# Kernel optimization log

Hardware: AMD Instinct MI355X
Metric: run time of the kernel (lower is better)

The kernel has to match this reference:

```python
import jax, jax.numpy as jnp
import numpy as np

# dims / constants (from init_kwargs and ParamsHP defaults)
N, C, TRS, SPT, BUF = 800, 64, 40, 10, 120
DT = 1e-4                      # step_size
A, OMEGA, G = -0.5, 10.0, 500.0
STD_IN, CY0, Y0_OFF, KG, KI = 100.0, 5.0, 2.0, 5.0, 1.0
T = TRS * SPT                  # total integration steps


def setup_inputs() -> dict:
    key = jax.random.key(0)
    k = jax.random.split(key, 7)
    external = jax.random.normal(k[0], (N, SPT, TRS), dtype=jnp.float32)
    hx = jax.random.uniform(k[1], (N, 2), dtype=jnp.float32)
    hE = jax.random.uniform(k[2], (N, BUF), dtype=jnp.float32)
    sc = jax.random.uniform(k[3], (N, N), dtype=jnp.float32)
    lm = jax.random.normal(k[4], (C, N), dtype=jnp.float32)
    noise_in = jax.random.normal(k[5], (T, N, 2), dtype=jnp.float32)
    # delays[i,j] = int(dist[i,j] / mu), bounded by buffer length
    delays = jax.random.randint(k[6], (N, N), 0, BUF, dtype=jnp.int64)
    return {"external": external, "hx": hx, "hE": hE, "sc": sc,
            "lm": lm, "noise_in": noise_in, "delays": delays}


def reference(external, hx, hE, sc, lm, noise_in, delays):
    # normalized structural connectivity and Laplacian diagonal term
    w = jnp.abs(sc)
    w_n = w / jnp.linalg.norm(w)          # (N,N)
    rowsum = jnp.sum(w_n, axis=1)         # (N,) -> dg = -diag(rowsum)
    jcol = jnp.broadcast_to(jnp.arange(N)[None, :], (N, N))
    # stimulus as (T, N): external is (N, steps_per_TR, TRs_per_window)
    ext = jnp.transpose(external, (2, 1, 0)).reshape(T, N)
    sqdt = jnp.sqrt(DT)

    def step(carry, inp):
        x, y, hEb = carry                 # x,y: (N,), hEb: (N,BUF)
        u, ns = inp                       # u: (N,), ns: (N,2)
        # delayed activity: Ed[i,j] = x_j(t - delays[i,j])
        Ed = hEb[jcol, delays]            # (N,N) irregular gather
        LEd = jnp.sum(w_n * Ed, axis=1)   # connectivity-weighted coupling
        r2 = x * x + y * y
        dx = (A - r2) * x - OMEGA * y + G * (LEd - rowsum * x) + KG * KI * u
        dy = (A - r2) * y + OMEGA * x
        x_new = x + DT * dx + sqdt * STD_IN * ns[:, 0]
        y_new = y + DT * dy + sqdt * STD_IN * ns[:, 1]
        hEb = jnp.concatenate([x_new[:, None], hEb[:, :-1]], axis=1)
        return (x_new, y_new, hEb), x_new

    (xf, yf, hEf), xs = jax.lax.scan(step, (hx[:, 0], hx[:, 1], hE), (ext, noise_in))
    # one EEG sample per TR (state at the last step of each TR)
    x_tr = xs.reshape(TRS, SPT, N)[:, -1, :]   # (TRS, N)
    eeg = CY0 * (x_tr @ lm.T) - Y0_OFF          # leadfield projection (TRS, C)
    return eeg.T                                # (C, TRS)
```

## Files before the change

### kernel.cpp

```cpp
#include <hip/hip_runtime.h>
#include <hip/hip_cooperative_groups.h>

namespace cg = cooperative_groups;

#define N_      800
#define C_      64
#define TRS_    40
#define SPT_    10
#define BUF_    120
#define T_      400
#define STRIDE  528
#define KPL     13
#define SENT    0x7FC00BADu
#define NEAR_D  15

#define A_F     (-0.5f)
#define OMEGA_F (10.0f)
#define G_F     (500.0f)
#define KGI_F   (5.0f)
#define DT_F    (1e-4f)

#define ALD(p)    __hip_atomic_load((p), __ATOMIC_RELAXED, __HIP_MEMORY_SCOPE_AGENT)
#define AST(p,v)  __hip_atomic_store((p), (v), __ATOMIC_RELAXED, __HIP_MEMORY_SCOPE_AGENT)


__global__ void k_sumsq(const float* __restrict__ sc, float* __restrict__ sumsq) {
    __shared__ float sh[4];
    int tid = threadIdx.x;
    int idx = blockIdx.x * 256 + tid;
    float s = 0.f;
    for (int i = idx; i < N_ * N_; i += 256 * 256) { float v = sc[i]; s += v * v; }
    #pragma unroll
    for (int o = 1; o < 64; o <<= 1) s += __shfl_xor(s, o, 64);
    if ((tid & 63) == 0) sh[tid >> 6] = s;
    __syncthreads();
    if (tid == 0) atomicAdd(sumsq, sh[0] + sh[1] + sh[2] + sh[3]);
}

__global__ void k_detect(const int* __restrict__ dw, int* __restrict__ flag) {
    __shared__ int sh[4];
    int tid = threadIdx.x;
    int v = 0;
    for (int idx = 2 * tid + 1; idx < 800; idx += 512) v |= dw[idx];
    #pragma unroll
    for (int o = 1; o < 64; o <<= 1) v |= __shfl_xor(v, o, 64);
    if ((tid & 63) == 0) sh[tid >> 6] = v;
    __syncthreads();
    if (tid == 0) flag[0] = ((sh[0] | sh[1] | sh[2] | sh[3]) == 0) ? 1 : 0;
}

__global__ void k_init(const float* __restrict__ hE, unsigned int* __restrict__ xh) {
    int idx = blockIdx.x * 256 + threadIdx.x;
    if (idx >= N_ * 520) return;
    int j = idx / 520, s = idx - j * 520;
    unsigned int v = (s < 120) ? __float_as_uint(hE[j * BUF_ + (119 - s)]) : SENT;
    xh[j * STRIDE + s] = v;
}


__global__ void __launch_bounds__(512, 1) k_main(
    const float* __restrict__ sc, const int* __restrict__ dw,
    const float* __restrict__ hx, const float* __restrict__ external,
    const float* __restrict__ noise, const float* __restrict__ lm,
    const float* __restrict__ sumsq, const int* __restrict__ flag,
    unsigned int* __restrict__ xh, float* __restrict__ xtr, float* __restrict__ out)
{
    cg::grid_group grid = cg::this_grid();
    const int lane = threadIdx.x & 63;
    const int i = (int)((blockIdx.x * 512 + threadIdx.x) >> 6);

    const float inv_norm = 1.0f / sqrtf(*sumsq);
    const int is64 = *flag;

    float wn[KPL], wf[KPL]; int an[KPL], af[KPL];
    float rsum = 0.f;
    #pragma unroll
    for (int k = 0; k < KPL; ++k) {
        int j = k * 64 + lane;
        bool valid = (j < N_);
        int jj = valid ? j : 0;
        int base = i * N_ + jj;
        float wv = valid ? fabsf(sc[base]) * inv_norm : 0.f;
        int dv = valid ? dw[is64 ? (base << 1) : base] : 119;
        rsum += wv;
        bool nearc = valid && (dv < NEAR_D);
        bool farc  = valid && (dv >= NEAR_D);
        wn[k] = nearc ? wv : 0.f;
        wf[k] = farc  ? wv : 0.f;
        an[k] = jj * STRIDE + 119 - (nearc ? dv : 119);
        af[k] = jj * STRIDE + 119 - (farc  ? dv : 119);
    }
    #pragma unroll
    for (int o = 1; o < 64; o <<= 1) rsum += __shfl_xor(rsum, o, 64);

    float x = hx[2 * i], y = hx[2 * i + 1];

    #pragma unroll 1
    for (int mb = 0; mb < 25; ++mb) {
        const int t0 = mb * 16;

        float fps[16];
        #pragma unroll
        for (int s = 0; s < 16; ++s) fps[s] = 0.f;

        #pragma unroll
        for (int k = 0; k < KPL; ++k) {
            bool fm = (wf[k] != 0.f);
            int a = af[k] + t0;
            int p = a & 3;
            int A = a - p;
            float4 q0, q1, q2, q3, q4;
            if (fm) {
                const float4* f4 = reinterpret_cast<const float4*>((const float*)xh + A);
                q0 = f4[0]; q1 = f4[1]; q2 = f4[2]; q3 = f4[3]; q4 = f4[4];
            } else {
                q0 = q1 = q2 = q3 = q4 = make_float4(0.f, 0.f, 0.f, 0.f);
            }
            float win[20] = { q0.x,q0.y,q0.z,q0.w, q1.x,q1.y,q1.z,q1.w,
                              q2.x,q2.y,q2.z,q2.w, q3.x,q3.y,q3.z,q3.w,
                              q4.x,q4.y,q4.z,q4.w };
            int g = 0;
            while (true) {
                int pend = 0;
                #pragma unroll
                for (int z = 0; z < 20; ++z)
                    pend |= (int)((z >= p) & (z < p + 16) &
                                  (__float_as_uint(win[z]) == SENT));
                if (!__any(pend)) break;
                if (++g > 1000000) break;
                #pragma unroll
                for (int z = 0; z < 20; ++z)
                    if ((z >= p) && (z < p + 16) && __float_as_uint(win[z]) == SENT)
                        win[z] = __uint_as_float(ALD(&xh[A + z]));
            }
            float wk = wf[k];
            #pragma unroll
            for (int s = 0; s < 16; ++s) {
                float v01 = (p & 1) ? win[s + 1] : win[s];
                float v23 = (p & 1) ? win[s + 3] : win[s + 2];
                float v   = (p & 2) ? v23 : v01;
                fps[s] += wk * v;
            }
        }

        #pragma unroll
        for (int s = 0; s < 16; ++s) {
            const int t = t0 + s;
            int tr = (t * 205) >> 11;
            int sp = t - tr * 10;
            float u  = external[(i * SPT_ + sp) * TRS_ + tr];
            float n0 = noise[(t * N_ + i) * 2 + 0];
            float n1 = noise[(t * N_ + i) * 2 + 1];

            unsigned vv[KPL];
            #pragma unroll
            for (int k = 0; k < KPL; ++k)
                vv[k] = (wn[k] != 0.f) ? ALD(&xh[an[k] + t]) : 0u;
            int g = 0;
            while (true) {
                int pend = 0;
                #pragma unroll
                for (int k = 0; k < KPL; ++k) pend |= (vv[k] == SENT) ? 1 : 0;
                if (!__any(pend)) break;
                if (++g > 1000000) break;
                #pragma unroll
                for (int k = 0; k < KPL; ++k)
                    if (vv[k] == SENT) vv[k] = ALD(&xh[an[k] + t]);
            }
            float acc = fps[s];
            #pragma unroll
            for (int k = 0; k < KPL; ++k) acc += wn[k] * __uint_as_float(vv[k]);
            #pragma unroll
            for (int o = 1; o < 64; o <<= 1) acc += __shfl_xor(acc, o, 64);

            float r2 = x * x + y * y;
            float dx = (A_F - r2) * x - OMEGA_F * y + G_F * (acc - rsum * x) + KGI_F * u;
            float dy = (A_F - r2) * y + OMEGA_F * x;
            x = x + DT_F * dx + n0;
            y = y + DT_F * dy + n1;

            if (lane == 0) {
                AST(&xh[i * STRIDE + 120 + t], __float_as_uint(x));
                if (sp == SPT_ - 1) xtr[tr * N_ + i] = x;
            }
        }
    }

    grid.sync();

    for (int o = i; o < C_ * TRS_; o += 800) {
        int c = o / TRS_, tr = o - c * TRS_;
        float s = 0.f;
        #pragma unroll
        for (int k = 0; k < KPL; ++k) {
            int n = k * 64 + lane;
            if (n < N_) s += xtr[tr * N_ + n] * lm[c * N_ + n];
        }
        #pragma unroll
        for (int o2 = 1; o2 < 64; o2 <<= 1) s += __shfl_xor(s, o2, 64);
        if (lane == 0) out[o] = 5.0f * s - 2.0f;
    }
}


extern "C" void kernel_launch(void* const* d_in, const int* in_sizes, int n_in,
                              void* d_out, int out_size, void* d_ws, size_t ws_size,
                              hipStream_t stream) {
    const float* external = (const float*)d_in[0];
    const float* hx       = (const float*)d_in[1];
    const float* hE       = (const float*)d_in[2];
    const float* sc       = (const float*)d_in[3];
    const float* lm       = (const float*)d_in[4];
    const float* noise    = (const float*)d_in[5];
    const int*   delays   = (const int*)  d_in[6];
    float* out = (float*)d_out;

    float*        sumsq = (float*)d_ws;
    int*          flag  = (int*)d_ws + 1;
    unsigned int* xh    = (unsigned int*)d_ws + 64;
    float*        xtr   = (float*)(xh + N_ * STRIDE);

    hipMemsetAsync(d_ws, 0, 8, stream);
    k_sumsq<<<256, 256, 0, stream>>>(sc, sumsq);
    k_detect<<<1, 256, 0, stream>>>(delays, flag);
    k_init<<<(N_ * 520 + 255) / 256, 256, 0, stream>>>(hE, xh);

    void* args[] = { (void*)&sc, (void*)&delays, (void*)&hx, (void*)&external,
                     (void*)&noise, (void*)&lm, (void*)&sumsq, (void*)&flag,
                     (void*)&xh, (void*)&xtr, (void*)&out };
    hipLaunchCooperativeKernel((const void*)k_main, dim3(100), dim3(512), args, 0, stream);
}
```

Before: 2.727 ms.

## Transpose history buffer and stage recent states in a shared-memory ring

The global history buffer is transposed to time-major layout, so each time step's 800 states are contiguous. Each block cooperatively pulls the previous step's full state vector into a 16-deep LDS ring, and near-delay connections read from LDS instead of issuing per-lane global atomic polls. Far-delay reads become strided per-element loads instead of float4 windows. This adds a block-wide __syncthreads and an 800-element global poll per step in every block.

```diff
diff --git a/kernel.cpp b/kernel.cpp
--- a/kernel.cpp
+++ b/kernel.cpp
@@ -9,10 +9,11 @@
 #define SPT_    10
 #define BUF_    120
 #define T_      400
-#define STRIDE  528
+#define ROWS_   520
 #define KPL     13
 #define SENT    0x7FC00BADu
-#define NEAR_D  15
+#define NEAR_D  16
+#define DEPTH   16
 
 #define A_F     (-0.5f)
 #define OMEGA_F (10.0f)
@@ -49,30 +50,35 @@
     if (tid == 0) flag[0] = ((sh[0] | sh[1] | sh[2] | sh[3]) == 0) ? 1 : 0;
 }
 
-__global__ void k_init(const float* __restrict__ hE, unsigned int* __restrict__ xh) {
+__global__ void k_init(const float* __restrict__ hE, unsigned int* __restrict__ xhT) {
     int idx = blockIdx.x * 256 + threadIdx.x;
-    if (idx >= N_ * 520) return;
-    int j = idx / 520, s = idx - j * 520;
-    unsigned int v = (s < 120) ? __float_as_uint(hE[j * BUF_ + (119 - s)]) : SENT;
-    xh[j * STRIDE + s] = v;
+    if (idx >= ROWS_ * N_) return;
+    int r = idx / N_, j = idx - r * N_;
+    unsigned int v = (r < 120) ? __float_as_uint(hE[j * BUF_ + (119 - r)]) : SENT;
+    xhT[r * N_ + j] = v;
 }
 
 
 __global__ void __launch_bounds__(512, 1) k_main(
     const float* __restrict__ sc, const int* __restrict__ dw,
-    const float* __restrict__ hx, const float* __restrict__ external,
-    const float* __restrict__ noise, const float* __restrict__ lm,
+    const float* __restrict__ hx, const float* __restrict__ hE,
+    const float* __restrict__ external, const float* __restrict__ noise,
+    const float* __restrict__ lm,
     const float* __restrict__ sumsq, const int* __restrict__ flag,
-    unsigned int* __restrict__ xh, float* __restrict__ xtr, float* __restrict__ out)
+    unsigned int* __restrict__ xhT, float* __restrict__ xtr, float* __restrict__ out)
 {
     cg::grid_group grid = cg::this_grid();
-    const int lane = threadIdx.x & 63;
-    const int i = (int)((blockIdx.x * 512 + threadIdx.x) >> 6);
+    __shared__ float ring[DEPTH * N_];
+
+    const int tid  = threadIdx.x;
+    const int lane = tid & 63;
+    const int wid  = tid >> 6;
+    const int i    = blockIdx.x * 8 + wid;
 
     const float inv_norm = 1.0f / sqrtf(*sumsq);
     const int is64 = *flag;
 
-    float wn[KPL], wf[KPL]; int an[KPL], af[KPL];
+    float wn[KPL], wf[KPL]; int dnn[KPL], jb[KPL], f0[KPL];
     float rsum = 0.f;
     #pragma unroll
     for (int k = 0; k < KPL; ++k) {
@@ -85,15 +91,22 @@
         rsum += wv;
         bool nearc = valid && (dv < NEAR_D);
         bool farc  = valid && (dv >= NEAR_D);
-        wn[k] = nearc ? wv : 0.f;
-        wf[k] = farc  ? wv : 0.f;
-        an[k] = jj * STRIDE + 119 - (nearc ? dv : 119);
-        af[k] = jj * STRIDE + 119 - (farc  ? dv : 119);
+        wn[k]  = nearc ? wv : 0.f;
+        dnn[k] = nearc ? dv : 0;
+        wf[k]  = farc  ? wv : 0.f;
+        int dvf = farc ? dv : 119;
+        f0[k]  = (119 - dvf) * N_ + jj;
+        jb[k]  = jj;
     }
     #pragma unroll
     for (int o = 1; o < 64; o <<= 1) rsum += __shfl_xor(rsum, o, 64);
 
     float x = hx[2 * i], y = hx[2 * i + 1];
+
+    for (int slot = 0; slot < DEPTH; ++slot)
+        for (int j = tid; j < N_; j += 512)
+            ring[slot * N_ + j] = hE[j * BUF_ + (15 - slot)];
+    __syncthreads();
 
     #pragma unroll 1
     for (int mb = 0; mb < 25; ++mb) {
@@ -105,42 +118,27 @@
 
         #pragma unroll
         for (int k = 0; k < KPL; ++k) {
-            bool fm = (wf[k] != 0.f);
-            int a = af[k] + t0;
-            int p = a & 3;
-            int A = a - p;
-            float4 q0, q1, q2, q3, q4;
-            if (fm) {
-                const float4* f4 = reinterpret_cast<const float4*>((const float*)xh + A);
-                q0 = f4[0]; q1 = f4[1]; q2 = f4[2]; q3 = f4[3]; q4 = f4[4];
-            } else {
-                q0 = q1 = q2 = q3 = q4 = make_float4(0.f, 0.f, 0.f, 0.f);
-            }
-            float win[20] = { q0.x,q0.y,q0.z,q0.w, q1.x,q1.y,q1.z,q1.w,
-                              q2.x,q2.y,q2.z,q2.w, q3.x,q3.y,q3.z,q3.w,
-                              q4.x,q4.y,q4.z,q4.w };
+            int base = f0[k] + t0 * N_;
+            float v[16];
+            #pragma unroll
+            for (int s = 0; s < 16; ++s)
+                v[s] = __uint_as_float(xhT[base + s * N_]);
             int g = 0;
             while (true) {
                 int pend = 0;
                 #pragma unroll
-                for (int z = 0; z < 20; ++z)
-                    pend |= (int)((z >= p) & (z < p + 16) &
-                                  (__float_as_uint(win[z]) == SENT));
+                for (int s = 0; s < 16; ++s)
+                    pend |= (__float_as_uint(v[s]) == SENT) ? 1 : 0;
                 if (!__any(pend)) break;
-                if (++g > 1000000) break;
+                if (++g > 2000000) break;
                 #pragma unroll
-                for (int z = 0; z < 20; ++z)
-                    if ((z >= p) && (z < p + 16) && __float_as_uint(win[z]) == SENT)
-                        win[z] = __uint_as_float(ALD(&xh[A + z]));
+                for (int s = 0; s < 16; ++s)
+                    if (__float_as_uint(v[s]) == SENT)
+                        v[s] = __uint_as_float(ALD(&xhT[base + s * N_]));
             }
             float wk = wf[k];
             #pragma unroll
-            for (int s = 0; s < 16; ++s) {
-                float v01 = (p & 1) ? win[s + 1] : win[s];
-                float v23 = (p & 1) ? win[s + 3] : win[s + 2];
-                float v   = (p & 2) ? v23 : v01;
-                fps[s] += wk * v;
-            }
+            for (int s = 0; s < 16; ++s) fps[s] += wk * v[s];
         }
 
         #pragma unroll
@@ -152,24 +150,27 @@
             float n0 = noise[(t * N_ + i) * 2 + 0];
             float n1 = noise[(t * N_ + i) * 2 + 1];
 
-            unsigned vv[KPL];
-            #pragma unroll
-            for (int k = 0; k < KPL; ++k)
-                vv[k] = (wn[k] != 0.f) ? ALD(&xh[an[k] + t]) : 0u;
-            int g = 0;
-            while (true) {
-                int pend = 0;
-                #pragma unroll
-                for (int k = 0; k < KPL; ++k) pend |= (vv[k] == SENT) ? 1 : 0;
-                if (!__any(pend)) break;
-                if (++g > 1000000) break;
-                #pragma unroll
-                for (int k = 0; k < KPL; ++k)
-                    if (vv[k] == SENT) vv[k] = ALD(&xh[an[k] + t]);
-            }
+            if (t > 0) {
+                const unsigned* fp = xhT + (t - 1 + 120) * N_;
+                unsigned c0 = ALD(&fp[tid]);
+                while (c0 == SENT) c0 = ALD(&fp[tid]);
+                unsigned c1 = 0;
+                if (tid < N_ - 512) {
+                    c1 = ALD(&fp[512 + tid]);
+                    while (c1 == SENT) c1 = ALD(&fp[512 + tid]);
+                }
+                float* rw = ring + ((t - 1) & 15) * N_;
+                rw[tid] = __uint_as_float(c0);
+                if (tid < N_ - 512) rw[512 + tid] = __uint_as_float(c1);
+            }
+            __syncthreads();
+
             float acc = fps[s];
             #pragma unroll
-            for (int k = 0; k < KPL; ++k) acc += wn[k] * __uint_as_float(vv[k]);
+            for (int k = 0; k < KPL; ++k) {
+                int sl = (t - 1 - dnn[k]) & 15;
+                acc += wn[k] * ring[sl * N_ + jb[k]];
+            }
             #pragma unroll
             for (int o = 1; o < 64; o <<= 1) acc += __shfl_xor(acc, o, 64);
 
@@ -180,7 +181,7 @@
             y = y + DT_F * dy + n1;
 
             if (lane == 0) {
-                AST(&xh[i * STRIDE + 120 + t], __float_as_uint(x));
+                AST(&xhT[(t + 120) * N_ + i], __float_as_uint(x));
                 if (sp == SPT_ - 1) xtr[tr * N_ + i] = x;
             }
         }
@@ -217,16 +218,17 @@
 
     float*        sumsq = (float*)d_ws;
     int*          flag  = (int*)d_ws + 1;
-    unsigned int* xh    = (unsigned int*)d_ws + 64;
-    float*        xtr   = (float*)(xh + N_ * STRIDE);
+    unsigned int* xhT   = (unsigned int*)d_ws + 64;
+    float*        xtr   = (float*)(xhT + ROWS_ * N_);
 
     hipMemsetAsync(d_ws, 0, 8, stream);
     k_sumsq<<<256, 256, 0, stream>>>(sc, sumsq);
     k_detect<<<1, 256, 0, stream>>>(delays, flag);
-    k_init<<<(N_ * 520 + 255) / 256, 256, 0, stream>>>(hE, xh);
-
-    void* args[] = { (void*)&sc, (void*)&delays, (void*)&hx, (void*)&external,
-                     (void*)&noise, (void*)&lm, (void*)&sumsq, (void*)&flag,
-                     (void*)&xh, (void*)&xtr, (void*)&out };
+    k_init<<<(ROWS_ * N_ + 255) / 256, 256, 0, stream>>>(hE, xhT);
+
+    void* args[] = { (void*)&sc, (void*)&delays, (void*)&hx, (void*)&hE,
+                     (void*)&external, (void*)&noise, (void*)&lm,
+                     (void*)&sumsq, (void*)&flag,
+                     (void*)&xhT, (void*)&xtr, (void*)&out };
     hipLaunchCooperativeKernel((const void*)k_main, dim3(100), dim3(512), args, 0, stream);
 }
```

New measurement: 2.800 ms. 2.7% more time.
